# Kernel optimization log

Hardware: AMD Instinct MI355X
Metric: run time of the kernel (lower is better)

The kernel has to match this reference:

```python
import jax, jax.numpy as jnp
import numpy as np

K = 10  # kNN neighbors (class default)
EPS = 1e-5


def _bn(h, g, b):
    # BatchNorm1d in training mode: batch statistics over the node/edge dim
    m = h.mean(axis=0, keepdims=True)
    v = jnp.var(h, axis=0, keepdims=True)
    return (h - m) * jax.lax.rsqrt(v + EPS) * g + b


def _edge_conv(x, B, w0, b0, g0, be0, w1, b1, g1, be1):
    # DynamicEdgeConv: kNN in feature space per graph, msg = MLP([x_i, x_j - x_i]), max-aggregate
    T, D = x.shape
    N = T // B
    xb = x.reshape(B, N, D)
    sq = jnp.sum(xb * xb, axis=-1)                              # [B,N]
    d2 = sq[:, :, None] + sq[:, None, :] - 2.0 * jnp.einsum('bnd,bmd->bnm', xb, xb)
    _, idx = jax.lax.top_k(-d2, K)                               # [B,N,K] (self included, dist 0)
    neigh = jax.vmap(lambda xg, ig: xg[ig])(xb, idx)             # [B,N,K,D]
    xi = jnp.broadcast_to(xb[:, :, None, :], neigh.shape)
    e = jnp.concatenate([xi, neigh - xi], axis=-1).reshape(T * K, 2 * D)
    h = _bn(jax.nn.relu(e @ w0 + b0), g0, be0)
    h = _bn(jax.nn.relu(h @ w1 + b1), g1, be1)
    return h.reshape(B, N, K, -1).max(axis=2).reshape(T, -1)     # [T,64]


def _forward(x,
             c1_w0, c1_b0, c1_g0, c1_be0, c1_w1, c1_b1, c1_g1, c1_be1,
             c2_w0, c2_b0, c2_g0, c2_be0, c2_w1, c2_b1, c2_g1, c2_be1,
             c3_w0, c3_b0, c3_g0, c3_be0, c3_w1, c3_b1, c3_g1, c3_be1,
             l1_w, l1_b, l1_g, l1_be,
             m0_w, m0_b, m0_g, m0_be,
             m1_w, m1_b, m1_g, m1_be,
             m2_w, m2_b, B):
    x1 = _edge_conv(x,  B, c1_w0, c1_b0, c1_g0, c1_be0, c1_w1, c1_b1, c1_g1, c1_be1)
    x2 = _edge_conv(x1, B, c2_w0, c2_b0, c2_g0, c2_be0, c2_w1, c2_b1, c2_g1, c2_be1)
    x3 = _edge_conv(x2, B, c3_w0, c3_b0, c3_g0, c3_be0, c3_w1, c3_b1, c3_g1, c3_be1)
    cat = jnp.concatenate([x1, x2, x3], axis=1)                  # [T,192]
    x4 = _bn(jax.nn.relu(cat @ l1_w + l1_b), l1_g, l1_be)        # [T,1024]
    N = x.shape[0] // B
    pooled = x4.reshape(B, N, -1).max(axis=1)                    # global_max_pool -> [B,1024]
    x5 = jnp.repeat(pooled, N, axis=0)                           # repeat per node -> [T,1024]
    h = jnp.concatenate([x1, x2, x3, x5], axis=1)                # [T,1216]
    h = _bn(jax.nn.relu(h @ m0_w + m0_b), m0_g, m0_be)
    h = _bn(jax.nn.relu(h @ m1_w + m1_b), m1_g, m1_be)
    return h @ m2_w + m2_b                                       # [T,1]


def setup_inputs() -> dict:
    key = jax.random.key(0)
    ks = iter(jax.random.split(key, 64))
    w = lambda s: jax.random.normal(next(ks), s, jnp.float32) * 0.05
    z = lambda c: jnp.zeros((c,), jnp.float32)
    o = lambda c: jnp.ones((c,), jnp.float32)
    d = {"x": jax.random.normal(next(ks), (16384, 6), jnp.float32)}
    # conv1: MLP([12,64,64]); conv2/conv3: MLP([128,64,64])
    for name, cin in (("c1", 12), ("c2", 128), ("c3", 128)):
        d[name + "_w0"], d[name + "_b0"], d[name + "_g0"], d[name + "_be0"] = w((cin, 64)), z(64), o(64), z(64)
        d[name + "_w1"], d[name + "_b1"], d[name + "_g1"], d[name + "_be1"] = w((64, 64)), z(64), o(64), z(64)
    d["l1_w"], d["l1_b"], d["l1_g"], d["l1_be"] = w((192, 1024)), z(1024), o(1024), z(1024)
    d["m0_w"], d["m0_b"], d["m0_g"], d["m0_be"] = w((1216, 256)), z(256), o(256), z(256)
    d["m1_w"], d["m1_b"], d["m1_g"], d["m1_be"] = w((256, 128)), z(128), o(128), z(128)
    d["m2_w"], d["m2_b"] = w((128, 1)), z(1)
    d["batch_size"] = 8
    return d


def reference(x,
              c1_w0, c1_b0, c1_g0, c1_be0, c1_w1, c1_b1, c1_g1, c1_be1,
              c2_w0, c2_b0, c2_g0, c2_be0, c2_w1, c2_b1, c2_g1, c2_be1,
              c3_w0, c3_b0, c3_g0, c3_be0, c3_w1, c3_b1, c3_g1, c3_be1,
              l1_w, l1_b, l1_g, l1_be,
              m0_w, m0_b, m0_g, m0_be,
              m1_w, m1_b, m1_g, m1_be,
              m2_w, m2_b, batch_size):
    return _forward(x,
                    c1_w0, c1_b0, c1_g0, c1_be0, c1_w1, c1_b1, c1_g1, c1_be1,
                    c2_w0, c2_b0, c2_g0, c2_be0, c2_w1, c2_b1, c2_g1, c2_be1,
                    c3_w0, c3_b0, c3_g0, c3_be0, c3_w1, c3_b1, c3_g1, c3_be1,
                    l1_w, l1_b, l1_g, l1_be,
                    m0_w, m0_b, m0_g, m0_be,
                    m1_w, m1_b, m1_g, m1_be,
                    m2_w, m2_b, int(batch_size))
```

## Files before the change

### kernel.cpp

```cpp
#include <hip/hip_runtime.h>
#include <stdint.h>


constexpr int T  = 16384;
constexpr int NBG = 8;
constexpr int NN = 2048;
constexpr int KK = 10;
constexpr float BN_EPS = 1e-5f;

__device__ __forceinline__ unsigned fkey(float f) {
  unsigned u = __float_as_uint(f);
  return (u & 0x80000000u) ? ~u : (u | 0x80000000u);
}
__device__ __forceinline__ float funkey(unsigned k) {
  unsigned u = (k & 0x80000000u) ? (k ^ 0x80000000u) : ~k;
  return __uint_as_float(u);
}

__device__ __forceinline__ void ins10(unsigned long long (&b)[KK],
                                      unsigned long long v) {
  b[KK - 1] = v;
#pragma unroll
  for (int s = KK - 1; s > 0; --s)
    if (b[s] < b[s - 1]) {
      unsigned long long t2 = b[s]; b[s] = b[s - 1]; b[s - 1] = t2;
    }
}

__global__ void zero_kernel(float* __restrict__ stats,
                            unsigned* __restrict__ cmax, unsigned* __restrict__ cmin) {
  const int gid = blockIdx.x * blockDim.x + threadIdx.x;
  if (gid < 9 * 2048) stats[gid] = 0.f;
  if (gid < NBG * 1024) { cmax[gid] = 0u; cmin[gid] = 0xFFFFFFFFu; }
}

__global__ void row_sq_kernel(const float* __restrict__ X, int ldx, int D,
                              float* __restrict__ sq) {
  const int t = blockIdx.x * blockDim.x + threadIdx.x;
  if (t >= T) return;
  const float* xr = X + (size_t)t * ldx;
  float s = 0.f;
  for (int d = 0; d < D; ++d) s = fmaf(xr[d], xr[d], s);
  sq[t] = s;
}

template<int D>
__global__ __launch_bounds__(256) void knn_kernel_t(
    const float* __restrict__ X, int ldx,
    const float* __restrict__ sq,
    unsigned long long* __restrict__ part ) {
  constexpr int R = (D == 64) ? 2 : 1;
  constexpr int ROWS = 16 * R;
  constexpr int BK = (D == 64) ? 8 : 6;
  constexpr int AF = D * ROWS;
  constexpr int BF = BK * 576;
  __shared__ __align__(16) float smem[AF + BF + 576];
  float* As = smem;
  float* Bs = smem + AF;
  float* sqs = smem + AF + BF;

  const int tid = threadIdx.x;
  const int blk = blockIdx.x;
  constexpr int BPG = (NN / ROWS) * 2;
  const int b = blk / BPG;
  const int rem = blk % BPG;
  const int ib = rem >> 1, jh = rem & 1;
  const int i0 = b * NN + ib * ROWS;
  const int jg0 = b * NN + jh * 1024;
  const int tg = tid >> 4, tc = tid & 15;

  if constexpr (D == 64) {
    const int r = tid & 31, ks = (tid >> 5) * 8;
    const float* rp = &X[(size_t)(i0 + r) * ldx + ks];
    const float4 v0 = *(const float4*)rp;
    const float4 v1 = *(const float4*)(rp + 4);
    As[(ks + 0) * ROWS + r] = v0.x; As[(ks + 1) * ROWS + r] = v0.y;
    As[(ks + 2) * ROWS + r] = v0.z; As[(ks + 3) * ROWS + r] = v0.w;
    As[(ks + 4) * ROWS + r] = v1.x; As[(ks + 5) * ROWS + r] = v1.y;
    As[(ks + 6) * ROWS + r] = v1.z; As[(ks + 7) * ROWS + r] = v1.w;
  } else {
    const int r = tid & 15, k = tid >> 4;
    if (k < D) As[k * ROWS + r] = X[(size_t)(i0 + r) * ldx + k];
  }

  const float FINF = __int_as_float(0x7F800000);
  float bk[R][KK]; int bj[R][KK];
  float thr[R], rowThr[R];
#pragma unroll
  for (int rr = 0; rr < R; ++rr) {
#pragma unroll
    for (int s = 0; s < KK; ++s) { bk[rr][s] = FINF; bj[rr][s] = 0; }
    thr[rr] = FINF; rowThr[rr] = FINF;
  }

  for (int jt = 0; jt < 2; ++jt) {
    const int jtbase = jg0 + jt * 512;
    float acc[R][32];
#pragma unroll
    for (int rr = 0; rr < R; ++rr)
#pragma unroll
      for (int c = 0; c < 32; ++c) acc[rr][c] = 0.f;

    if constexpr (D == 64) {
      for (int kb = 0; kb < 64; kb += 8) {
        __syncthreads();
#pragma unroll
        for (int h = 0; h < 2; ++h) {
          const int c = tid + h * 256;
          const float* rp = &X[(size_t)(jtbase + c) * ldx + kb];
          const float4 v0 = *(const float4*)rp;
          const float4 v1 = *(const float4*)(rp + 4);
          const int co = (c >> 5) * 36 + (c & 31);
          Bs[0 * 576 + co] = v0.x; Bs[1 * 576 + co] = v0.y;
          Bs[2 * 576 + co] = v0.z; Bs[3 * 576 + co] = v0.w;
          Bs[4 * 576 + co] = v1.x; Bs[5 * 576 + co] = v1.y;
          Bs[6 * 576 + co] = v1.z; Bs[7 * 576 + co] = v1.w;
          if (kb == 0) sqs[co] = sq[jtbase + c];
        }
        __syncthreads();
#pragma unroll
        for (int kk = 0; kk < 8; ++kk) {
          float a[R];
#pragma unroll
          for (int rr = 0; rr < R; ++rr)
            a[rr] = As[(kb + kk) * ROWS + R * tg + rr];
          const float* bp = &Bs[kk * 576 + tc * 36];
#pragma unroll
          for (int c4 = 0; c4 < 8; ++c4) {
            const float4 bv = *(const float4*)(bp + c4 * 4);
#pragma unroll
            for (int rr = 0; rr < R; ++rr) {
              acc[rr][c4 * 4 + 0] = fmaf(a[rr], bv.x, acc[rr][c4 * 4 + 0]);
              acc[rr][c4 * 4 + 1] = fmaf(a[rr], bv.y, acc[rr][c4 * 4 + 1]);
              acc[rr][c4 * 4 + 2] = fmaf(a[rr], bv.z, acc[rr][c4 * 4 + 2]);
              acc[rr][c4 * 4 + 3] = fmaf(a[rr], bv.w, acc[rr][c4 * 4 + 3]);
            }
          }
        }
      }
    } else {
      __syncthreads();
#pragma unroll
      for (int h = 0; h < 2; ++h) {
        const int c = tid + h * 256;
        const float* rp = &X[(size_t)(jtbase + c) * ldx];
        const int co = (c >> 5) * 36 + (c & 31);
#pragma unroll
        for (int k = 0; k < 6; ++k) Bs[k * 576 + co] = rp[k];
        sqs[co] = sq[jtbase + c];
      }
      __syncthreads();
#pragma unroll
      for (int kk = 0; kk < 6; ++kk) {
        const float a0 = As[kk * ROWS + tg];
        const float* bp = &Bs[kk * 576 + tc * 36];
#pragma unroll
        for (int c4 = 0; c4 < 8; ++c4) {
          const float4 bv = *(const float4*)(bp + c4 * 4);
          acc[0][c4 * 4 + 0] = fmaf(a0, bv.x, acc[0][c4 * 4 + 0]);
          acc[0][c4 * 4 + 1] = fmaf(a0, bv.y, acc[0][c4 * 4 + 1]);
          acc[0][c4 * 4 + 2] = fmaf(a0, bv.z, acc[0][c4 * 4 + 2]);
          acc[0][c4 * 4 + 3] = fmaf(a0, bv.w, acc[0][c4 * 4 + 3]);
        }
      }
    }

#pragma unroll
    for (int c4 = 0; c4 < 8; ++c4) {
      const float4 sv = *(const float4*)&sqs[tc * 36 + c4 * 4];
      const float svv[4] = {sv.x, sv.y, sv.z, sv.w};
#pragma unroll
      for (int u = 0; u < 4; ++u) {
        const int c = c4 * 4 + u;
        const int j = jtbase + tc * 32 + c;
#pragma unroll
        for (int rr = 0; rr < R; ++rr) {
          const float m = fmaf(-2.f, acc[rr][c], svv[u]);
          if (m <= rowThr[rr] && m < thr[rr]) {
            bk[rr][KK - 1] = m; bj[rr][KK - 1] = j;
#pragma unroll
            for (int s = KK - 1; s > 0; --s) {
              const bool sw = bk[rr][s] < bk[rr][s - 1];
              const float ka = bk[rr][s - 1], kb2 = bk[rr][s];
              bk[rr][s - 1] = sw ? kb2 : ka; bk[rr][s] = sw ? ka : kb2;
              const int ja = bj[rr][s - 1], jb2 = bj[rr][s];
              bj[rr][s - 1] = sw ? jb2 : ja; bj[rr][s] = sw ? ja : jb2;
            }
            thr[rr] = bk[rr][KK - 1];
          }
        }
      }
    }
#pragma unroll
    for (int rr = 0; rr < R; ++rr) {
      float r0 = thr[rr];
#pragma unroll
      for (int d = 1; d < 16; d <<= 1) r0 = fminf(r0, __shfl_xor(r0, d, 64));
      rowThr[rr] = r0;
    }
  }

  unsigned long long* o =
      part + ((size_t)(i0 + R * tg + tc) * 2 + jh) * KK;
#pragma unroll
  for (int s = 0; s < KK; ++s) {
#pragma unroll
    for (int rr = 0; rr < R; ++rr) {
      float w = bk[rr][0];
#pragma unroll
      for (int d = 1; d < 16; d <<= 1) w = fminf(w, __shfl_xor(w, d, 64));
      int cj = (bk[rr][0] == w) ? bj[rr][0] : 0x7FFFFFFF;
#pragma unroll
      for (int d = 1; d < 16; d <<= 1) {
        const int oc = __shfl_xor(cj, d, 64);
        cj = (oc < cj) ? oc : cj;
      }
      const bool pop = (bk[rr][0] == w) && (bj[rr][0] == cj);
#pragma unroll
      for (int q = 0; q < KK - 1; ++q) {
        bk[rr][q] = pop ? bk[rr][q + 1] : bk[rr][q];
        bj[rr][q] = pop ? bj[rr][q + 1] : bj[rr][q];
      }
      if (pop) bk[rr][KK - 1] = FINF;
      if (tc == rr)
        o[s] = ((unsigned long long)fkey(w) << 32) | (unsigned)cj;
    }
  }
}

__global__ void knn_merge2_kernel(const unsigned long long* __restrict__ part,
                                  int* __restrict__ idx) {
  const int i = blockIdx.x * blockDim.x + threadIdx.x;
  if (i >= T) return;
  const unsigned long long* p = part + (size_t)i * 2 * KK;
  unsigned long long best[KK];
#pragma unroll
  for (int s = 0; s < KK; ++s) best[s] = ~0ULL;
  for (int q = 0; q < 2 * KK; ++q) {
    const unsigned long long v = p[q];
    if (v < best[KK - 1]) ins10(best, v);
  }
#pragma unroll
  for (int s = 0; s < KK; ++s) idx[i * KK + s] = (int)(best[s] & 0xffffffffu);
}

__global__ void wprep_kernel(const float* __restrict__ w0,
                             const float* __restrict__ b0, int D,
                             float* __restrict__ wp, float* __restrict__ bp) {
  const int gid = blockIdx.x * blockDim.x + threadIdx.x;
  if (gid < D * 128) {
    const int d = gid >> 7, c = gid & 127;
    wp[gid] = (c < 64) ? (w0[d * 64 + c] - w0[(D + d) * 64 + c])
                       : w0[(D + d) * 64 + (c - 64)];
  } else if (gid < D * 128 + 128) {
    const int c = gid - D * 128;
    bp[c] = (c < 64) ? b0[c] : 0.f;
  }
}

__global__ void nodegemm6_kernel(const float* __restrict__ X,
                                 const float* __restrict__ wp,
                                 const float* __restrict__ bp,
                                 float* __restrict__ hb) {
  const int tid = threadIdx.x;
  const int c = tid & 127;
  const int t = blockIdx.x * 2 + (tid >> 7);
  const float* xr = X + (size_t)t * 6;
  float v = bp[c];
#pragma unroll
  for (int d = 0; d < 6; ++d) v = fmaf(xr[d], wp[d * 128 + c], v);
  hb[(size_t)t * 128 + c] = v;
}

__global__ __launch_bounds__(256) void stat0_kernel(
    const float* __restrict__ hb, const int* __restrict__ idx,
    float* __restrict__ stat) {
  const int wv = threadIdx.x >> 6, lane = threadIdx.x & 63;
  const int e0 = (blockIdx.x * 4 + wv) * 16;
  float s1 = 0.f, s2 = 0.f;
  for (int q = 0; q < 16; ++q) {
    const int e = e0 + q;
    const int t = e / 10;
    const int jg = idx[e];
    const float v = fmaxf(hb[(size_t)t * 128 + lane] +
                          hb[(size_t)jg * 128 + 64 + lane], 0.f);
    s1 += v; s2 = fmaf(v, v, s2);
  }
  __shared__ float ls[4][64];
  ls[wv][lane] = s1;
  __syncthreads();
  if (wv == 0) atomicAdd(&stat[lane], ls[0][lane] + ls[1][lane] + ls[2][lane] + ls[3][lane]);
  __syncthreads();
  ls[wv][lane] = s2;
  __syncthreads();
  if (wv == 0) atomicAdd(&stat[1024 + lane], ls[0][lane] + ls[1][lane] + ls[2][lane] + ls[3][lane]);
}

__global__ void fold_kernel(const float* __restrict__ stat, float cntInv,
                            const float* __restrict__ g, const float* __restrict__ be,
                            const float* __restrict__ W, const float* __restrict__ bias,
                            float* __restrict__ Wf, float* __restrict__ bf,
                            int Cin, int Cout) {
  const int gid = blockIdx.x * blockDim.x + threadIdx.x;
  const int nW = Cin * Cout;
  if (gid < nW) {
    const int d = gid / Cout;
    const float mean = stat[d] * cntInv;
    const float var = fmaf(-mean, mean, stat[1024 + d] * cntInv);
    const float a = g[d] * rsqrtf(var + BN_EPS);
    Wf[gid] = a * W[gid];
  } else if (gid < nW + Cout) {
    const int j = gid - nW;
    float acc = bias[j];
    for (int d = 0; d < Cin; ++d) {
      const float mean = stat[d] * cntInv;
      const float var = fmaf(-mean, mean, stat[1024 + d] * cntInv);
      const float a = g[d] * rsqrtf(var + BN_EPS);
      const float c = fmaf(-mean, a, be[d]);
      acc = fmaf(c, W[d * Cout + j], acc);
    }
    bf[j] = acc;
  }
}

__global__ __launch_bounds__(256) void mlp1n_kernel(
    const float* __restrict__ hb, const int* __restrict__ idx,
    const float* __restrict__ w1f, const float* __restrict__ b1f,
    float* __restrict__ xmax, float* __restrict__ xmin,
    float* __restrict__ stat) {
  __shared__ __align__(16) float As[32 * 164];
  __shared__ __align__(16) float Bs[32][64];
  __shared__ int ids[160];
  __shared__ float red[16][64];
  const int tid = threadIdx.x;
  const int row0 = blockIdx.x * 160;
  const int tn = tid >> 4, tx = tid & 15;
  if (tid < 160) ids[tid] = idx[row0 + tid];
  float acc[10][4] = {};
  for (int kb = 0; kb < 64; kb += 32) {
    __syncthreads();
    for (int f = tid; f < 160 * 8; f += 256) {
      const int r = f >> 3, q = f & 7;
      const int t = blockIdx.x * 16 + r / 10;
      const int jg = ids[r];
      const float4 va = *(const float4*)&hb[(size_t)t * 128 + kb + q * 4];
      const float4 vb = *(const float4*)&hb[(size_t)jg * 128 + 64 + kb + q * 4];
      As[(q * 4 + 0) * 164 + r] = fmaxf(va.x + vb.x, 0.f);
      As[(q * 4 + 1) * 164 + r] = fmaxf(va.y + vb.y, 0.f);
      As[(q * 4 + 2) * 164 + r] = fmaxf(va.z + vb.z, 0.f);
      As[(q * 4 + 3) * 164 + r] = fmaxf(va.w + vb.w, 0.f);
    }
    {
      const int kr = tid >> 4, c4 = tid & 15;
#pragma unroll
      for (int h = 0; h < 2; ++h) {
        const int k2 = kr + h * 16;
        *(float4*)&Bs[k2][c4 * 4] =
            *(const float4*)&w1f[(size_t)(kb + k2) * 64 + c4 * 4];
      }
    }
    __syncthreads();
#pragma unroll
    for (int k = 0; k < 32; ++k) {
      const float* ap = &As[k * 164 + tn * 10];
      const float4 bv = *(const float4*)&Bs[k][tx * 4];
#pragma unroll
      for (int i = 0; i < 10; ++i) {
        const float a = ap[i];
        acc[i][0] = fmaf(a, bv.x, acc[i][0]);
        acc[i][1] = fmaf(a, bv.y, acc[i][1]);
        acc[i][2] = fmaf(a, bv.z, acc[i][2]);
        acc[i][3] = fmaf(a, bv.w, acc[i][3]);
      }
    }
  }
  const int node = blockIdx.x * 16 + tn;
  float s2v[4];
#pragma unroll
  for (int j = 0; j < 4; ++j) {
    const float bj = b1f[tx * 4 + j];
    float mx = -3.4e38f, mn = 3.4e38f, s1 = 0.f, s2 = 0.f;
#pragma unroll
    for (int i = 0; i < 10; ++i) {
      const float v = fmaxf(acc[i][j] + bj, 0.f);
      mx = fmaxf(mx, v); mn = fminf(mn, v);
      s1 += v; s2 = fmaf(v, v, s2);
    }
    xmax[(size_t)node * 64 + tx * 4 + j] = mx;
    xmin[(size_t)node * 64 + tx * 4 + j] = mn;
    red[tn][tx * 4 + j] = s1;
    s2v[j] = s2;
  }
  __syncthreads();
  if (tid < 64) {
    float s = 0.f;
#pragma unroll
    for (int q = 0; q < 16; ++q) s += red[q][tid];
    atomicAdd(&stat[tid], s);
  }
  __syncthreads();
#pragma unroll
  for (int j = 0; j < 4; ++j) red[tn][tx * 4 + j] = s2v[j];
  __syncthreads();
  if (tid < 64) {
    float s = 0.f;
#pragma unroll
    for (int q = 0; q < 16; ++q) s += red[q][tid];
    atomicAdd(&stat[1024 + tid], s);
  }
}

__global__ void conv_out_kernel(const float* __restrict__ xmax, const float* __restrict__ xmin,
                                const float* __restrict__ stat, float cntInv,
                                const float* __restrict__ g, const float* __restrict__ be,
                                float* __restrict__ cat, int coff) {
  const int gid = blockIdx.x * blockDim.x + threadIdx.x;
  const int c = gid & 63, t = gid >> 6;
  const float mean = stat[c] * cntInv;
  const float var = fmaf(-mean, mean, stat[1024 + c] * cntInv);
  const float a = g[c] * rsqrtf(var + BN_EPS);
  const float cc = fmaf(-mean, a, be[c]);
  const float v = (a >= 0.f) ? fmaf(a, xmax[gid], cc) : fmaf(a, xmin[gid], cc);
  cat[(size_t)t * 192 + coff + c] = v;
}

__global__ __launch_bounds__(256) void gemm_kernel(
    const float* __restrict__ A, int lda,
    const float* __restrict__ Bw, int ldb,
    const float* __restrict__ bias, int biasPerGraph,
    float* __restrict__ C,
    float* __restrict__ stat,
    unsigned* __restrict__ cmax, unsigned* __restrict__ cmin,
    int Kdim, int Ncols, int doRelu) {
  __shared__ float As[32][68];
  __shared__ float Bs[32][64];
  const int tid = threadIdx.x;
  const int nbx = Ncols >> 6;
  const int bx = blockIdx.x % nbx, by = blockIdx.x / nbx;
  const int row0 = by << 6, col0 = bx << 6;
  const int tx = tid & 15, ty = tid >> 4;
  float acc[4][4] = {};
  for (int kb = 0; kb < Kdim; kb += 32) {
    __syncthreads();
    {
      const int r = tid >> 3, fc = tid & 7;
#pragma unroll
      for (int h = 0; h < 2; ++h) {
        const int rr = r + h * 32;
        const float4 va = *(const float4*)&A[(size_t)(row0 + rr) * lda + kb + fc * 4];
        As[fc * 4 + 0][rr] = va.x; As[fc * 4 + 1][rr] = va.y;
        As[fc * 4 + 2][rr] = va.z; As[fc * 4 + 3][rr] = va.w;
      }
      const int kr = tid >> 4, c4 = tid & 15;
#pragma unroll
      for (int h = 0; h < 2; ++h) {
        const int k2 = kr + h * 16;
        *(float4*)&Bs[k2][c4 * 4] =
            *(const float4*)&Bw[(size_t)(kb + k2) * ldb + col0 + c4 * 4];
      }
    }
    __syncthreads();
#pragma unroll
    for (int k = 0; k < 32; ++k) {
      const float4 av = *(const float4*)&As[k][ty * 4];
      const float4 bv = *(const float4*)&Bs[k][tx * 4];
      const float a4[4] = {av.x, av.y, av.z, av.w};
      const float b4[4] = {bv.x, bv.y, bv.z, bv.w};
#pragma unroll
      for (int i = 0; i < 4; ++i)
#pragma unroll
        for (int j = 0; j < 4; ++j) acc[i][j] = fmaf(a4[i], b4[j], acc[i][j]);
    }
  }
  const int graph = row0 >> 11;
  const float* bp = bias + (biasPerGraph ? graph * Ncols : 0) + col0 + tx * 4;
  float v[4][4];
#pragma unroll
  for (int j = 0; j < 4; ++j) {
    const float bj = bp[j];
#pragma unroll
    for (int i = 0; i < 4; ++i) {
      const float s = acc[i][j] + bj;
      v[i][j] = doRelu ? fmaxf(s, 0.f) : s;
    }
  }
  if (C) {
#pragma unroll
    for (int i = 0; i < 4; ++i) {
      const float4 st = make_float4(v[i][0], v[i][1], v[i][2], v[i][3]);
      *(float4*)&C[(size_t)(row0 + ty * 4 + i) * Ncols + col0 + tx * 4] = st;
    }
  }
  if (stat) {
    __syncthreads();
#pragma unroll
    for (int j = 0; j < 4; ++j)
      As[ty][tx * 4 + j] = v[0][j] + v[1][j] + v[2][j] + v[3][j];
    __syncthreads();
    if (tid < 64) {
      float s = 0.f;
#pragma unroll
      for (int q = 0; q < 16; ++q) s += As[q][tid];
      atomicAdd(&stat[col0 + tid], s);
    }
    __syncthreads();
#pragma unroll
    for (int j = 0; j < 4; ++j) {
      float s = 0.f;
#pragma unroll
      for (int i = 0; i < 4; ++i) s = fmaf(v[i][j], v[i][j], s);
      As[ty][tx * 4 + j] = s;
    }
    __syncthreads();
    if (tid < 64) {
      float s = 0.f;
#pragma unroll
      for (int q = 0; q < 16; ++q) s += As[q][tid];
      atomicAdd(&stat[1024 + col0 + tid], s);
    }
    if (cmax) {
      __syncthreads();
#pragma unroll
      for (int j = 0; j < 4; ++j)
        As[ty][tx * 4 + j] = fmaxf(fmaxf(v[0][j], v[1][j]), fmaxf(v[2][j], v[3][j]));
      __syncthreads();
      if (tid < 64) {
        float s = As[0][tid];
#pragma unroll
        for (int q = 1; q < 16; ++q) s = fmaxf(s, As[q][tid]);
        atomicMax(&cmax[graph * Ncols + col0 + tid], fkey(s));
      }
      __syncthreads();
#pragma unroll
      for (int j = 0; j < 4; ++j)
        As[ty][tx * 4 + j] = fminf(fminf(v[0][j], v[1][j]), fminf(v[2][j], v[3][j]));
      __syncthreads();
      if (tid < 64) {
        float s = As[0][tid];
#pragma unroll
        for (int q = 1; q < 16; ++q) s = fminf(s, As[q][tid]);
        atomicMin(&cmin[graph * Ncols + col0 + tid], fkey(s));
      }
    }
  }
}

__global__ void pool_finalize_kernel(const unsigned* __restrict__ cmax,
                                     const unsigned* __restrict__ cmin,
                                     const float* __restrict__ stat, float cntInv,
                                     const float* __restrict__ g, const float* __restrict__ be,
                                     float* __restrict__ pooled) {
  const int gid = blockIdx.x * blockDim.x + threadIdx.x;
  if (gid >= NBG * 1024) return;
  const int col = gid & 1023;
  const float mean = stat[col] * cntInv;
  const float var = fmaf(-mean, mean, stat[1024 + col] * cntInv);
  const float a = g[col] * rsqrtf(var + BN_EPS);
  const float cc = fmaf(-mean, a, be[col]);
  const float fx = funkey(cmax[gid]), fn = funkey(cmin[gid]);
  pooled[gid] = (a >= 0.f) ? fmaf(a, fx, cc) : fmaf(a, fn, cc);
}

__global__ void po_gemm_kernel(const float* __restrict__ pooled,
                               const float* __restrict__ w2,
                               const float* __restrict__ m0b,
                               float* __restrict__ po) {
  const int b = blockIdx.x, j = threadIdx.x;
  const float* pr = pooled + b * 1024;
  float a0 = m0b[j], a1 = 0.f, a2 = 0.f, a3 = 0.f;
  for (int d = 0; d < 1024; d += 4) {
    a0 = fmaf(pr[d + 0], w2[(size_t)(d + 0) * 256 + j], a0);
    a1 = fmaf(pr[d + 1], w2[(size_t)(d + 1) * 256 + j], a1);
    a2 = fmaf(pr[d + 2], w2[(size_t)(d + 2) * 256 + j], a2);
    a3 = fmaf(pr[d + 3], w2[(size_t)(d + 3) * 256 + j], a3);
  }
  po[b * 256 + j] = (a0 + a1) + (a2 + a3);
}

__global__ __launch_bounds__(256) void m2_gemv_kernel(
    const float* __restrict__ hm1, const float* __restrict__ m2f,
    const float* __restrict__ m2fb, float* __restrict__ out) {
  const int wv = threadIdx.x >> 6, lane = threadIdx.x & 63;
  const int t = blockIdx.x * 4 + wv;
  const float* r = hm1 + (size_t)t * 128;
  float v = fmaf(r[lane], m2f[lane], r[64 + lane] * m2f[64 + lane]);
  for (int off = 32; off; off >>= 1) v += __shfl_down(v, off);
  if (lane == 0) out[t] = v + m2fb[0];
}

extern "C" void kernel_launch(void* const* d_in, const int* in_sizes, int n_in,
                              void* d_out, int out_size, void* d_ws, size_t ws_size,
                              hipStream_t stream) {
  const float* x = (const float*)d_in[0];
  const float* c_w0[3] = {(const float*)d_in[1], (const float*)d_in[9],  (const float*)d_in[17]};
  const float* c_b0[3] = {(const float*)d_in[2], (const float*)d_in[10], (const float*)d_in[18]};
  const float* c_g0[3] = {(const float*)d_in[3], (const float*)d_in[11], (const float*)d_in[19]};
  const float* c_be0[3]= {(const float*)d_in[4], (const float*)d_in[12], (const float*)d_in[20]};
  const float* c_w1[3] = {(const float*)d_in[5], (const float*)d_in[13], (const float*)d_in[21]};
  const float* c_b1[3] = {(const float*)d_in[6], (const float*)d_in[14], (const float*)d_in[22]};
  const float* c_g1[3] = {(const float*)d_in[7], (const float*)d_in[15], (const float*)d_in[23]};
  const float* c_be1[3]= {(const float*)d_in[8], (const float*)d_in[16], (const float*)d_in[24]};
  const float* l1_w = (const float*)d_in[25];
  const float* l1_b = (const float*)d_in[26];
  const float* l1_g = (const float*)d_in[27];
  const float* l1_be= (const float*)d_in[28];
  const float* m0_w = (const float*)d_in[29];
  const float* m0_b = (const float*)d_in[30];
  const float* m0_g = (const float*)d_in[31];
  const float* m0_be= (const float*)d_in[32];
  const float* m1_w = (const float*)d_in[33];
  const float* m1_b = (const float*)d_in[34];
  const float* m1_g = (const float*)d_in[35];
  const float* m1_be= (const float*)d_in[36];
  const float* m2_w = (const float*)d_in[37];
  const float* m2_b = (const float*)d_in[38];
  float* out = (float*)d_out;

  char* ws = (char*)d_ws;
  float*    stats  = (float*)(ws + 0);
  unsigned* cmax   = (unsigned*)(ws + 73728);
  unsigned* cmin   = (unsigned*)(ws + 106496);
  float*    pooled = (float*)(ws + 139264);
  float*    po     = (float*)(ws + 172032);
  float*    w1f    = (float*)(ws + 180224);
  float*    b1f    = (float*)(ws + 196608);
  float*    m1f    = (float*)(ws + 196864);
  float*    m1fb   = (float*)(ws + 327936);
  float*    m2f    = (float*)(ws + 328448);
  float*    m2fb   = (float*)(ws + 328960);
  float*    sq     = (float*)(ws + 329216);
  int*      idx    = (int*)  (ws + 394752);
  float*    xmax   = (float*)(ws + 1050112);
  float*    xmin   = (float*)(ws + 5244416);
  float*    cat    = (float*)(ws + 9438720);
  float*    wp[3]  = {(float*)(ws + 22021632),
                      (float*)(ws + 22025216),
                      (float*)(ws + 22058496)};
  float*    bp[3]  = {(float*)(ws + 22024704), (float*)(ws + 22057984),
                      (float*)(ws + 22091264)};
  char*     regA   = ws + 22091776;
  unsigned long long* part = (unsigned long long*)regA;
  float*    hb     = (float*)(regA + 2621440);
  float*    hm0    = (float*)regA;
  float*    hm1    = (float*)(regA + 16777216);

  const float cInvE = 1.f / (float)(T * KK);
  const float cInvT = 1.f / (float)T;

  zero_kernel<<<72, 256, 0, stream>>>(stats, cmax, cmin);
  wprep_kernel<<<4, 256, 0, stream>>>(c_w0[0], c_b0[0], 6, wp[0], bp[0]);
  wprep_kernel<<<33, 256, 0, stream>>>(c_w0[1], c_b0[1], 64, wp[1], bp[1]);
  wprep_kernel<<<33, 256, 0, stream>>>(c_w0[2], c_b0[2], 64, wp[2], bp[2]);

  for (int cidx = 0; cidx < 3; ++cidx) {
    const float* Xin; int ldx, Din;
    const int coff = cidx * 64;
    if (cidx == 0) { Xin = x; ldx = 6; Din = 6; }
    else { Xin = cat + (cidx - 1) * 64; ldx = 192; Din = 64; }
    float* st0 = stats + (cidx * 2) * 2048;
    float* st1 = stats + (cidx * 2 + 1) * 2048;

    row_sq_kernel<<<T / 256, 256, 0, stream>>>(Xin, ldx, Din, sq);
    if (Din == 6)
      knn_kernel_t<6><<<2048, 256, 0, stream>>>(Xin, ldx, sq, part);
    else
      knn_kernel_t<64><<<1024, 256, 0, stream>>>(Xin, ldx, sq, part);
    knn_merge2_kernel<<<T / 256, 256, 0, stream>>>(part, idx);
    if (Din == 6)
      nodegemm6_kernel<<<T / 2, 256, 0, stream>>>(Xin, wp[0], bp[0], hb);
    else
      gemm_kernel<<<(T / 64) * 2, 256, 0, stream>>>(
          Xin, ldx, wp[cidx], 128, bp[cidx], 0, hb,
          nullptr, nullptr, nullptr, 64, 128, 0);
    stat0_kernel<<<T * KK / 64, 256, 0, stream>>>(hb, idx, st0);
    fold_kernel<<<17, 256, 0, stream>>>(st0, cInvE, c_g0[cidx], c_be0[cidx],
                                        c_w1[cidx], c_b1[cidx], w1f, b1f, 64, 64);
    mlp1n_kernel<<<T * KK / 160, 256, 0, stream>>>(hb, idx, w1f, b1f,
                                                   xmax, xmin, st1);
    conv_out_kernel<<<T * 64 / 256, 256, 0, stream>>>(xmax, xmin, st1, cInvE,
                                                      c_g1[cidx], c_be1[cidx], cat, coff);
  }

  float* stl1 = stats + 6 * 2048;
  gemm_kernel<<<(T / 64) * (1024 / 64), 256, 0, stream>>>(
      cat, 192, l1_w, 1024, l1_b, 0, nullptr, stl1, cmax, cmin, 192, 1024, 1);
  pool_finalize_kernel<<<32, 256, 0, stream>>>(cmax, cmin, stl1, cInvT, l1_g, l1_be, pooled);
  po_gemm_kernel<<<8, 256, 0, stream>>>(pooled, m0_w + 192 * 256, m0_b, po);

  float* stm0 = stats + 7 * 2048;
  gemm_kernel<<<(T / 64) * (256 / 64), 256, 0, stream>>>(
      cat, 192, m0_w, 256, po, 1, hm0, stm0, nullptr, nullptr, 192, 256, 1);
  fold_kernel<<<129, 256, 0, stream>>>(stm0, cInvT, m0_g, m0_be, m1_w, m1_b, m1f, m1fb, 256, 128);

  float* stm1 = stats + 8 * 2048;
  gemm_kernel<<<(T / 64) * (128 / 64), 256, 0, stream>>>(
      hm0, 256, m1f, 128, m1fb, 0, hm1, stm1, nullptr, nullptr, 256, 128, 1);
  fold_kernel<<<1, 256, 0, stream>>>(stm1, cInvT, m1_g, m1_be, m2_w, m2_b, m2f, m2fb, 128, 1);
  m2_gemv_kernel<<<T / 4, 256, 0, stream>>>(hm1, m2f, m2fb, out);
}
```

Baseline: 1.369 ms.

## Fuse row-norm into kNN tiles, merge prep launches, retile 64-dim kNN

```diff
diff --git a/kernel.cpp b/kernel.cpp
--- a/kernel.cpp
+++ b/kernel.cpp
@@ -27,227 +27,25 @@
     }
 }
 
-__global__ void zero_kernel(float* __restrict__ stats,
-                            unsigned* __restrict__ cmax, unsigned* __restrict__ cmin) {
-  const int gid = blockIdx.x * blockDim.x + threadIdx.x;
-  if (gid < 9 * 2048) stats[gid] = 0.f;
-  if (gid < NBG * 1024) { cmax[gid] = 0u; cmin[gid] = 0xFFFFFFFFu; }
-}
-
-__global__ void row_sq_kernel(const float* __restrict__ X, int ldx, int D,
-                              float* __restrict__ sq) {
-  const int t = blockIdx.x * blockDim.x + threadIdx.x;
-  if (t >= T) return;
-  const float* xr = X + (size_t)t * ldx;
-  float s = 0.f;
-  for (int d = 0; d < D; ++d) s = fmaf(xr[d], xr[d], s);
-  sq[t] = s;
-}
-
-template<int D>
-__global__ __launch_bounds__(256) void knn_kernel_t(
-    const float* __restrict__ X, int ldx,
-    const float* __restrict__ sq,
-    unsigned long long* __restrict__ part ) {
-  constexpr int R = (D == 64) ? 2 : 1;
-  constexpr int ROWS = 16 * R;
-  constexpr int BK = (D == 64) ? 8 : 6;
-  constexpr int AF = D * ROWS;
-  constexpr int BF = BK * 576;
-  __shared__ __align__(16) float smem[AF + BF + 576];
-  float* As = smem;
-  float* Bs = smem + AF;
-  float* sqs = smem + AF + BF;
-
-  const int tid = threadIdx.x;
-  const int blk = blockIdx.x;
-  constexpr int BPG = (NN / ROWS) * 2;
-  const int b = blk / BPG;
-  const int rem = blk % BPG;
-  const int ib = rem >> 1, jh = rem & 1;
-  const int i0 = b * NN + ib * ROWS;
-  const int jg0 = b * NN + jh * 1024;
-  const int tg = tid >> 4, tc = tid & 15;
-
-  if constexpr (D == 64) {
-    const int r = tid & 31, ks = (tid >> 5) * 8;
-    const float* rp = &X[(size_t)(i0 + r) * ldx + ks];
-    const float4 v0 = *(const float4*)rp;
-    const float4 v1 = *(const float4*)(rp + 4);
-    As[(ks + 0) * ROWS + r] = v0.x; As[(ks + 1) * ROWS + r] = v0.y;
-    As[(ks + 2) * ROWS + r] = v0.z; As[(ks + 3) * ROWS + r] = v0.w;
-    As[(ks + 4) * ROWS + r] = v1.x; As[(ks + 5) * ROWS + r] = v1.y;
-    As[(ks + 6) * ROWS + r] = v1.z; As[(ks + 7) * ROWS + r] = v1.w;
-  } else {
-    const int r = tid & 15, k = tid >> 4;
-    if (k < D) As[k * ROWS + r] = X[(size_t)(i0 + r) * ldx + k];
-  }
-
-  const float FINF = __int_as_float(0x7F800000);
-  float bk[R][KK]; int bj[R][KK];
-  float thr[R], rowThr[R];
-#pragma unroll
-  for (int rr = 0; rr < R; ++rr) {
-#pragma unroll
-    for (int s = 0; s < KK; ++s) { bk[rr][s] = FINF; bj[rr][s] = 0; }
-    thr[rr] = FINF; rowThr[rr] = FINF;
-  }
-
-  for (int jt = 0; jt < 2; ++jt) {
-    const int jtbase = jg0 + jt * 512;
-    float acc[R][32];
-#pragma unroll
-    for (int rr = 0; rr < R; ++rr)
-#pragma unroll
-      for (int c = 0; c < 32; ++c) acc[rr][c] = 0.f;
-
-    if constexpr (D == 64) {
-      for (int kb = 0; kb < 64; kb += 8) {
-        __syncthreads();
-#pragma unroll
-        for (int h = 0; h < 2; ++h) {
-          const int c = tid + h * 256;
-          const float* rp = &X[(size_t)(jtbase + c) * ldx + kb];
-          const float4 v0 = *(const float4*)rp;
-          const float4 v1 = *(const float4*)(rp + 4);
-          const int co = (c >> 5) * 36 + (c & 31);
-          Bs[0 * 576 + co] = v0.x; Bs[1 * 576 + co] = v0.y;
-          Bs[2 * 576 + co] = v0.z; Bs[3 * 576 + co] = v0.w;
-          Bs[4 * 576 + co] = v1.x; Bs[5 * 576 + co] = v1.y;
-          Bs[6 * 576 + co] = v1.z; Bs[7 * 576 + co] = v1.w;
-          if (kb == 0) sqs[co] = sq[jtbase + c];
-        }
-        __syncthreads();
-#pragma unroll
-        for (int kk = 0; kk < 8; ++kk) {
-          float a[R];
-#pragma unroll
-          for (int rr = 0; rr < R; ++rr)
-            a[rr] = As[(kb + kk) * ROWS + R * tg + rr];
-          const float* bp = &Bs[kk * 576 + tc * 36];
-#pragma unroll
-          for (int c4 = 0; c4 < 8; ++c4) {
-            const float4 bv = *(const float4*)(bp + c4 * 4);
-#pragma unroll
-            for (int rr = 0; rr < R; ++rr) {
-              acc[rr][c4 * 4 + 0] = fmaf(a[rr], bv.x, acc[rr][c4 * 4 + 0]);
-              acc[rr][c4 * 4 + 1] = fmaf(a[rr], bv.y, acc[rr][c4 * 4 + 1]);
-              acc[rr][c4 * 4 + 2] = fmaf(a[rr], bv.z, acc[rr][c4 * 4 + 2]);
-              acc[rr][c4 * 4 + 3] = fmaf(a[rr], bv.w, acc[rr][c4 * 4 + 3]);
-            }
-          }
-        }
-      }
-    } else {
-      __syncthreads();
-#pragma unroll
-      for (int h = 0; h < 2; ++h) {
-        const int c = tid + h * 256;
-        const float* rp = &X[(size_t)(jtbase + c) * ldx];
-        const int co = (c >> 5) * 36 + (c & 31);
-#pragma unroll
-        for (int k = 0; k < 6; ++k) Bs[k * 576 + co] = rp[k];
-        sqs[co] = sq[jtbase + c];
-      }
-      __syncthreads();
-#pragma unroll
-      for (int kk = 0; kk < 6; ++kk) {
-        const float a0 = As[kk * ROWS + tg];
-        const float* bp = &Bs[kk * 576 + tc * 36];
-#pragma unroll
-        for (int c4 = 0; c4 < 8; ++c4) {
-          const float4 bv = *(const float4*)(bp + c4 * 4);
-          acc[0][c4 * 4 + 0] = fmaf(a0, bv.x, acc[0][c4 * 4 + 0]);
-          acc[0][c4 * 4 + 1] = fmaf(a0, bv.y, acc[0][c4 * 4 + 1]);
-          acc[0][c4 * 4 + 2] = fmaf(a0, bv.z, acc[0][c4 * 4 + 2]);
-          acc[0][c4 * 4 + 3] = fmaf(a0, bv.w, acc[0][c4 * 4 + 3]);
-        }
-      }
-    }
-
-#pragma unroll
-    for (int c4 = 0; c4 < 8; ++c4) {
-      const float4 sv = *(const float4*)&sqs[tc * 36 + c4 * 4];
-      const float svv[4] = {sv.x, sv.y, sv.z, sv.w};
-#pragma unroll
-      for (int u = 0; u < 4; ++u) {
-        const int c = c4 * 4 + u;
-        const int j = jtbase + tc * 32 + c;
-#pragma unroll
-        for (int rr = 0; rr < R; ++rr) {
-          const float m = fmaf(-2.f, acc[rr][c], svv[u]);
-          if (m <= rowThr[rr] && m < thr[rr]) {
-            bk[rr][KK - 1] = m; bj[rr][KK - 1] = j;
-#pragma unroll
-            for (int s = KK - 1; s > 0; --s) {
-              const bool sw = bk[rr][s] < bk[rr][s - 1];
-              const float ka = bk[rr][s - 1], kb2 = bk[rr][s];
-              bk[rr][s - 1] = sw ? kb2 : ka; bk[rr][s] = sw ? ka : kb2;
-              const int ja = bj[rr][s - 1], jb2 = bj[rr][s];
-              bj[rr][s - 1] = sw ? jb2 : ja; bj[rr][s] = sw ? ja : jb2;
-            }
-            thr[rr] = bk[rr][KK - 1];
-          }
-        }
-      }
-    }
-#pragma unroll
-    for (int rr = 0; rr < R; ++rr) {
-      float r0 = thr[rr];
-#pragma unroll
-      for (int d = 1; d < 16; d <<= 1) r0 = fminf(r0, __shfl_xor(r0, d, 64));
-      rowThr[rr] = r0;
-    }
-  }
-
-  unsigned long long* o =
-      part + ((size_t)(i0 + R * tg + tc) * 2 + jh) * KK;
-#pragma unroll
-  for (int s = 0; s < KK; ++s) {
-#pragma unroll
-    for (int rr = 0; rr < R; ++rr) {
-      float w = bk[rr][0];
-#pragma unroll
-      for (int d = 1; d < 16; d <<= 1) w = fminf(w, __shfl_xor(w, d, 64));
-      int cj = (bk[rr][0] == w) ? bj[rr][0] : 0x7FFFFFFF;
-#pragma unroll
-      for (int d = 1; d < 16; d <<= 1) {
-        const int oc = __shfl_xor(cj, d, 64);
-        cj = (oc < cj) ? oc : cj;
-      }
-      const bool pop = (bk[rr][0] == w) && (bj[rr][0] == cj);
-#pragma unroll
-      for (int q = 0; q < KK - 1; ++q) {
-        bk[rr][q] = pop ? bk[rr][q + 1] : bk[rr][q];
-        bj[rr][q] = pop ? bj[rr][q + 1] : bj[rr][q];
-      }
-      if (pop) bk[rr][KK - 1] = FINF;
-      if (tc == rr)
-        o[s] = ((unsigned long long)fkey(w) << 32) | (unsigned)cj;
-    }
-  }
-}
-
-__global__ void knn_merge2_kernel(const unsigned long long* __restrict__ part,
-                                  int* __restrict__ idx) {
-  const int i = blockIdx.x * blockDim.x + threadIdx.x;
-  if (i >= T) return;
-  const unsigned long long* p = part + (size_t)i * 2 * KK;
-  unsigned long long best[KK];
-#pragma unroll
-  for (int s = 0; s < KK; ++s) best[s] = ~0ULL;
-  for (int q = 0; q < 2 * KK; ++q) {
-    const unsigned long long v = p[q];
-    if (v < best[KK - 1]) ins10(best, v);
-  }
-#pragma unroll
-  for (int s = 0; s < KK; ++s) idx[i * KK + s] = (int)(best[s] & 0xffffffffu);
-}
-
-__global__ void wprep_kernel(const float* __restrict__ w0,
-                             const float* __restrict__ b0, int D,
-                             float* __restrict__ wp, float* __restrict__ bp) {
-  const int gid = blockIdx.x * blockDim.x + threadIdx.x;
+__global__ void prep_kernel(float* __restrict__ stats,
+                            unsigned* __restrict__ cmax, unsigned* __restrict__ cmin,
+                            const float* __restrict__ w0a, const float* __restrict__ b0a,
+                            const float* __restrict__ w0b, const float* __restrict__ b0b,
+                            const float* __restrict__ w0c, const float* __restrict__ b0c,
+                            float* __restrict__ wpa, float* __restrict__ bpa,
+                            float* __restrict__ wpb, float* __restrict__ bpb,
+                            float* __restrict__ wpc, float* __restrict__ bpc) {
+  const int blk = blockIdx.x, tid = threadIdx.x;
+  if (blk < 72) {
+    const int gid = blk * 256 + tid;
+    if (gid < 9 * 2048) stats[gid] = 0.f;
+    if (gid < NBG * 1024) { cmax[gid] = 0u; cmin[gid] = 0xFFFFFFFFu; }
+    return;
+  }
+  const float* w0; const float* b0; float* wp; float* bp; int D, gid;
+  if (blk < 76)       { w0 = w0a; b0 = b0a; wp = wpa; bp = bpa; D = 6;  gid = (blk - 72) * 256 + tid; }
+  else if (blk < 109) { w0 = w0b; b0 = b0b; wp = wpb; bp = bpb; D = 64; gid = (blk - 76) * 256 + tid; }
+  else                { w0 = w0c; b0 = b0c; wp = wpc; bp = bpc; D = 64; gid = (blk - 109) * 256 + tid; }
   if (gid < D * 128) {
     const int d = gid >> 7, c = gid & 127;
     wp[gid] = (c < 64) ? (w0[d * 64 + c] - w0[(D + d) * 64 + c])
@@ -256,6 +54,305 @@
     const int c = gid - D * 128;
     bp[c] = (c < 64) ? b0[c] : 0.f;
   }
+}
+
+__global__ __launch_bounds__(256) void knn64_kernel(
+    const float* __restrict__ X, int ldx,
+    unsigned long long* __restrict__ part ) {
+  constexpr int AF = 64 * 16;
+  constexpr int BF = 8 * 576;
+  __shared__ __align__(16) float smem[AF + BF + 576];
+  float* As = smem;
+  float* Bs = smem + AF;
+  float* sqs = smem + AF + BF;
+
+  const int tid = threadIdx.x;
+  const int blk = blockIdx.x;
+  const int b = blk >> 8;
+  const int rem = blk & 255;
+  const int ib = rem >> 1, jh = rem & 1;
+  const int i0 = b * NN + ib * 16;
+  const int jg0 = b * NN + jh * 1024;
+  const int tg = tid >> 5, tc = tid & 31;
+
+  {
+    const int r = tid & 15, kq = tid >> 4;
+    const float4 v = *(const float4*)&X[(size_t)(i0 + r) * ldx + kq * 4];
+    As[(kq * 4 + 0) * 16 + r] = v.x; As[(kq * 4 + 1) * 16 + r] = v.y;
+    As[(kq * 4 + 2) * 16 + r] = v.z; As[(kq * 4 + 3) * 16 + r] = v.w;
+  }
+
+  const float FINF = __int_as_float(0x7F800000);
+  float bk0[KK], bk1[KK]; int bj0[KK], bj1[KK];
+#pragma unroll
+  for (int s = 0; s < KK; ++s) { bk0[s] = FINF; bj0[s] = 0; bk1[s] = FINF; bj1[s] = 0; }
+  float thr0 = FINF, thr1 = FINF, rowThr0 = FINF, rowThr1 = FINF;
+
+  for (int jt = 0; jt < 2; ++jt) {
+    const int jtbase = jg0 + jt * 512;
+    float acc0[16] = {}, acc1[16] = {};
+    float sqa0 = 0.f, sqa1 = 0.f;
+
+    for (int kb = 0; kb < 64; kb += 8) {
+      __syncthreads();
+#pragma unroll
+      for (int h = 0; h < 2; ++h) {
+        const int c = tid + h * 256;
+        const float* rp = &X[(size_t)(jtbase + c) * ldx + kb];
+        const float4 v0 = *(const float4*)rp;
+        const float4 v1 = *(const float4*)(rp + 4);
+        const int co = (c >> 4) * 18 + (c & 15);
+        Bs[0 * 576 + co] = v0.x; Bs[1 * 576 + co] = v0.y;
+        Bs[2 * 576 + co] = v0.z; Bs[3 * 576 + co] = v0.w;
+        Bs[4 * 576 + co] = v1.x; Bs[5 * 576 + co] = v1.y;
+        Bs[6 * 576 + co] = v1.z; Bs[7 * 576 + co] = v1.w;
+        float sq = v0.x * v0.x;
+        sq = fmaf(v0.y, v0.y, sq); sq = fmaf(v0.z, v0.z, sq);
+        sq = fmaf(v0.w, v0.w, sq); sq = fmaf(v1.x, v1.x, sq);
+        sq = fmaf(v1.y, v1.y, sq); sq = fmaf(v1.z, v1.z, sq);
+        sq = fmaf(v1.w, v1.w, sq);
+        if (h == 0) sqa0 += sq; else sqa1 += sq;
+        if (kb == 56) sqs[co] = (h == 0) ? sqa0 : sqa1;
+      }
+      __syncthreads();
+#pragma unroll
+      for (int kk = 0; kk < 8; ++kk) {
+        const float2 av = *(const float2*)&As[(kb + kk) * 16 + 2 * tg];
+        const float a0 = av.x, a1 = av.y;
+        const float* bp = &Bs[kk * 576 + tc * 18];
+#pragma unroll
+        for (int c4 = 0; c4 < 4; ++c4) {
+          const float4 bv = *(const float4*)(bp + c4 * 4);
+          acc0[c4 * 4 + 0] = fmaf(a0, bv.x, acc0[c4 * 4 + 0]);
+          acc0[c4 * 4 + 1] = fmaf(a0, bv.y, acc0[c4 * 4 + 1]);
+          acc0[c4 * 4 + 2] = fmaf(a0, bv.z, acc0[c4 * 4 + 2]);
+          acc0[c4 * 4 + 3] = fmaf(a0, bv.w, acc0[c4 * 4 + 3]);
+          acc1[c4 * 4 + 0] = fmaf(a1, bv.x, acc1[c4 * 4 + 0]);
+          acc1[c4 * 4 + 1] = fmaf(a1, bv.y, acc1[c4 * 4 + 1]);
+          acc1[c4 * 4 + 2] = fmaf(a1, bv.z, acc1[c4 * 4 + 2]);
+          acc1[c4 * 4 + 3] = fmaf(a1, bv.w, acc1[c4 * 4 + 3]);
+        }
+      }
+    }
+
+#pragma unroll
+    for (int c4 = 0; c4 < 4; ++c4) {
+      const float4 sv = *(const float4*)&sqs[tc * 18 + c4 * 4];
+      const float svv[4] = {sv.x, sv.y, sv.z, sv.w};
+#pragma unroll
+      for (int u = 0; u < 4; ++u) {
+        const int c = c4 * 4 + u;
+        const int j = jtbase + tc * 16 + c;
+        const float m0 = fmaf(-2.f, acc0[c], svv[u]);
+        if (m0 <= rowThr0 && m0 < thr0) {
+          bk0[KK - 1] = m0; bj0[KK - 1] = j;
+#pragma unroll
+          for (int s = KK - 1; s > 0; --s) {
+            const bool sw = bk0[s] < bk0[s - 1];
+            const float ka = bk0[s - 1], kb2 = bk0[s];
+            bk0[s - 1] = sw ? kb2 : ka; bk0[s] = sw ? ka : kb2;
+            const int ja = bj0[s - 1], jb2 = bj0[s];
+            bj0[s - 1] = sw ? jb2 : ja; bj0[s] = sw ? ja : jb2;
+          }
+          thr0 = bk0[KK - 1];
+        }
+        const float m1 = fmaf(-2.f, acc1[c], svv[u]);
+        if (m1 <= rowThr1 && m1 < thr1) {
+          bk1[KK - 1] = m1; bj1[KK - 1] = j;
+#pragma unroll
+          for (int s = KK - 1; s > 0; --s) {
+            const bool sw = bk1[s] < bk1[s - 1];
+            const float ka = bk1[s - 1], kb2 = bk1[s];
+            bk1[s - 1] = sw ? kb2 : ka; bk1[s] = sw ? ka : kb2;
+            const int ja = bj1[s - 1], jb2 = bj1[s];
+            bj1[s - 1] = sw ? jb2 : ja; bj1[s] = sw ? ja : jb2;
+          }
+          thr1 = bk1[KK - 1];
+        }
+      }
+    }
+    float r0 = thr0, r1 = thr1;
+#pragma unroll
+    for (int d = 1; d < 32; d <<= 1) {
+      r0 = fminf(r0, __shfl_xor(r0, d, 64));
+      r1 = fminf(r1, __shfl_xor(r1, d, 64));
+    }
+    rowThr0 = r0; rowThr1 = r1;
+  }
+
+#pragma unroll
+  for (int s = 0; s < KK; ++s) {
+    float w0 = bk0[0];
+#pragma unroll
+    for (int d = 1; d < 32; d <<= 1) w0 = fminf(w0, __shfl_xor(w0, d, 64));
+    int cj0 = (bk0[0] == w0) ? bj0[0] : 0x7FFFFFFF;
+#pragma unroll
+    for (int d = 1; d < 32; d <<= 1) {
+      const int oc = __shfl_xor(cj0, d, 64);
+      cj0 = (oc < cj0) ? oc : cj0;
+    }
+    const bool pop0 = (bk0[0] == w0) && (bj0[0] == cj0);
+#pragma unroll
+    for (int q = 0; q < KK - 1; ++q) {
+      bk0[q] = pop0 ? bk0[q + 1] : bk0[q];
+      bj0[q] = pop0 ? bj0[q + 1] : bj0[q];
+    }
+    if (pop0) bk0[KK - 1] = FINF;
+    if (tc == 0)
+      part[((size_t)(i0 + 2 * tg) * 2 + jh) * KK + s] =
+          ((unsigned long long)fkey(w0) << 32) | (unsigned)cj0;
+
+    float w1 = bk1[0];
+#pragma unroll
+    for (int d = 1; d < 32; d <<= 1) w1 = fminf(w1, __shfl_xor(w1, d, 64));
+    int cj1 = (bk1[0] == w1) ? bj1[0] : 0x7FFFFFFF;
+#pragma unroll
+    for (int d = 1; d < 32; d <<= 1) {
+      const int oc = __shfl_xor(cj1, d, 64);
+      cj1 = (oc < cj1) ? oc : cj1;
+    }
+    const bool pop1 = (bk1[0] == w1) && (bj1[0] == cj1);
+#pragma unroll
+    for (int q = 0; q < KK - 1; ++q) {
+      bk1[q] = pop1 ? bk1[q + 1] : bk1[q];
+      bj1[q] = pop1 ? bj1[q + 1] : bj1[q];
+    }
+    if (pop1) bk1[KK - 1] = FINF;
+    if (tc == 1)
+      part[((size_t)(i0 + 2 * tg + 1) * 2 + jh) * KK + s] =
+          ((unsigned long long)fkey(w1) << 32) | (unsigned)cj1;
+  }
+}
+
+__global__ __launch_bounds__(256) void knn6_kernel(
+    const float* __restrict__ X,
+    unsigned long long* __restrict__ part ) {
+  constexpr int AF = 6 * 16;
+  constexpr int BF = 6 * 576;
+  __shared__ __align__(16) float smem[AF + BF + 576];
+  float* As = smem;
+  float* Bs = smem + AF;
+  float* sqs = smem + AF + BF;
+
+  const int tid = threadIdx.x;
+  const int blk = blockIdx.x;
+  const int b = blk >> 8;
+  const int rem = blk & 255;
+  const int ib = rem >> 1, jh = rem & 1;
+  const int i0 = b * NN + ib * 16;
+  const int jg0 = b * NN + jh * 1024;
+  const int tg = tid >> 4, tc = tid & 15;
+
+  {
+    const int r = tid & 15, k = tid >> 4;
+    if (k < 6) As[k * 16 + r] = X[(size_t)(i0 + r) * 6 + k];
+  }
+
+  const float FINF = __int_as_float(0x7F800000);
+  float bk[KK]; int bj[KK];
+#pragma unroll
+  for (int s = 0; s < KK; ++s) { bk[s] = FINF; bj[s] = 0; }
+  float thr = FINF, rowThr = FINF;
+
+  for (int jt = 0; jt < 2; ++jt) {
+    const int jtbase = jg0 + jt * 512;
+    float acc[32] = {};
+    __syncthreads();
+#pragma unroll
+    for (int h = 0; h < 2; ++h) {
+      const int c = tid + h * 256;
+      const float* rp = &X[(size_t)(jtbase + c) * 6];
+      const int co = (c >> 5) * 36 + (c & 31);
+      float sq = 0.f;
+#pragma unroll
+      for (int k = 0; k < 6; ++k) {
+        const float v = rp[k];
+        Bs[k * 576 + co] = v;
+        sq = fmaf(v, v, sq);
+      }
+      sqs[co] = sq;
+    }
+    __syncthreads();
+#pragma unroll
+    for (int kk = 0; kk < 6; ++kk) {
+      const float a0 = As[kk * 16 + tg];
+      const float* bp = &Bs[kk * 576 + tc * 36];
+#pragma unroll
+      for (int c4 = 0; c4 < 8; ++c4) {
+        const float4 bv = *(const float4*)(bp + c4 * 4);
+        acc[c4 * 4 + 0] = fmaf(a0, bv.x, acc[c4 * 4 + 0]);
+        acc[c4 * 4 + 1] = fmaf(a0, bv.y, acc[c4 * 4 + 1]);
+        acc[c4 * 4 + 2] = fmaf(a0, bv.z, acc[c4 * 4 + 2]);
+        acc[c4 * 4 + 3] = fmaf(a0, bv.w, acc[c4 * 4 + 3]);
+      }
+    }
+#pragma unroll
+    for (int c4 = 0; c4 < 8; ++c4) {
+      const float4 sv = *(const float4*)&sqs[tc * 36 + c4 * 4];
+      const float svv[4] = {sv.x, sv.y, sv.z, sv.w};
+#pragma unroll
+      for (int u = 0; u < 4; ++u) {
+        const int c = c4 * 4 + u;
+        const int j = jtbase + tc * 32 + c;
+        const float m = fmaf(-2.f, acc[c], svv[u]);
+        if (m <= rowThr && m < thr) {
+          bk[KK - 1] = m; bj[KK - 1] = j;
+#pragma unroll
+          for (int s = KK - 1; s > 0; --s) {
+            const bool sw = bk[s] < bk[s - 1];
+            const float ka = bk[s - 1], kb2 = bk[s];
+            bk[s - 1] = sw ? kb2 : ka; bk[s] = sw ? ka : kb2;
+            const int ja = bj[s - 1], jb2 = bj[s];
+            bj[s - 1] = sw ? jb2 : ja; bj[s] = sw ? ja : jb2;
+          }
+          thr = bk[KK - 1];
+        }
+      }
+    }
+    float r0 = thr;
+#pragma unroll
+    for (int d = 1; d < 16; d <<= 1) r0 = fminf(r0, __shfl_xor(r0, d, 64));
+    rowThr = r0;
+  }
+
+  unsigned long long* o = part + ((size_t)(i0 + tg) * 2 + jh) * KK;
+#pragma unroll
+  for (int s = 0; s < KK; ++s) {
+    float w = bk[0];
+#pragma unroll
+    for (int d = 1; d < 16; d <<= 1) w = fminf(w, __shfl_xor(w, d, 64));
+    int cj = (bk[0] == w) ? bj[0] : 0x7FFFFFFF;
+#pragma unroll
+    for (int d = 1; d < 16; d <<= 1) {
+      const int oc = __shfl_xor(cj, d, 64);
+      cj = (oc < cj) ? oc : cj;
+    }
+    const bool pop = (bk[0] == w) && (bj[0] == cj);
+#pragma unroll
+    for (int q = 0; q < KK - 1; ++q) {
+      bk[q] = pop ? bk[q + 1] : bk[q];
+      bj[q] = pop ? bj[q + 1] : bj[q];
+    }
+    if (pop) bk[KK - 1] = FINF;
+    if (tc == 0)
+      o[s] = ((unsigned long long)fkey(w) << 32) | (unsigned)cj;
+  }
+}
+
+__global__ void knn_merge2_kernel(const unsigned long long* __restrict__ part,
+                                  int* __restrict__ idx) {
+  const int i = blockIdx.x * blockDim.x + threadIdx.x;
+  if (i >= T) return;
+  const unsigned long long* p = part + (size_t)i * 2 * KK;
+  unsigned long long best[KK];
+#pragma unroll
+  for (int s = 0; s < KK; ++s) best[s] = ~0ULL;
+  for (int q = 0; q < 2 * KK; ++q) {
+    const unsigned long long v = p[q];
+    if (v < best[KK - 1]) ins10(best, v);
+  }
+#pragma unroll
+  for (int s = 0; s < KK; ++s) idx[i * KK + s] = (int)(best[s] & 0xffffffffu);
 }
 
 __global__ void nodegemm6_kernel(const float* __restrict__ X,
@@ -628,7 +725,6 @@
   float*    m1fb   = (float*)(ws + 327936);
   float*    m2f    = (float*)(ws + 328448);
   float*    m2fb   = (float*)(ws + 328960);
-  float*    sq     = (float*)(ws + 329216);
   int*      idx    = (int*)  (ws + 394752);
   float*    xmax   = (float*)(ws + 1050112);
   float*    xmin   = (float*)(ws + 5244416);
@@ -647,10 +743,9 @@
   const float cInvE = 1.f / (float)(T * KK);
   const float cInvT = 1.f / (float)T;
 
-  zero_kernel<<<72, 256, 0, stream>>>(stats, cmax, cmin);
-  wprep_kernel<<<4, 256, 0, stream>>>(c_w0[0], c_b0[0], 6, wp[0], bp[0]);
-  wprep_kernel<<<33, 256, 0, stream>>>(c_w0[1], c_b0[1], 64, wp[1], bp[1]);
-  wprep_kernel<<<33, 256, 0, stream>>>(c_w0[2], c_b0[2], 64, wp[2], bp[2]);
+  prep_kernel<<<142, 256, 0, stream>>>(stats, cmax, cmin,
+                                       c_w0[0], c_b0[0], c_w0[1], c_b0[1], c_w0[2], c_b0[2],
+                                       wp[0], bp[0], wp[1], bp[1], wp[2], bp[2]);
 
   for (int cidx = 0; cidx < 3; ++cidx) {
     const float* Xin; int ldx, Din;
@@ -660,11 +755,10 @@
     float* st0 = stats + (cidx * 2) * 2048;
     float* st1 = stats + (cidx * 2 + 1) * 2048;
 
-    row_sq_kernel<<<T / 256, 256, 0, stream>>>(Xin, ldx, Din, sq);
     if (Din == 6)
-      knn_kernel_t<6><<<2048, 256, 0, stream>>>(Xin, ldx, sq, part);
+      knn6_kernel<<<2048, 256, 0, stream>>>(Xin, part);
     else
-      knn_kernel_t<64><<<1024, 256, 0, stream>>>(Xin, ldx, sq, part);
+      knn64_kernel<<<2048, 256, 0, stream>>>(Xin, ldx, part);
     knn_merge2_kernel<<<T / 256, 256, 0, stream>>>(part, idx);
     if (Din == 6)
       nodegemm6_kernel<<<T / 2, 256, 0, stream>>>(Xin, wp[0], bp[0], hb);
```

New measurement: 2.016 ms. 1.47x slower.
